# Performance work log

Measured on AMD Instinct MI355X. Metric: run time of the kernel, lower is better.

Reference implementation:

```python
import jax, jax.numpy as jnp
import numpy as np
import math

Q_SHAPES = [(20, 30), (10, 15), (5, 8)]
S_SHAPES = [(20, 30), (10, 15), (5, 8)]
C_IN = 256
C_OUT = 256
NUM_HEADS = 8


def _rel_indices(q_shapes, s_shapes):
    # Faithful translation of QSGA.get_rel_indices: block matrix over pyramid levels.
    rows = []
    for hq, wq in q_shapes:
        cols = []
        for hs, ws in s_shapes:
            ind = np.arange(ws)[None, :] / ws - np.arange(hq)[:, None] / hq  # [hq, ws]
            sc = math.sqrt(ws * hq)
            indx = np.tile(ind, (wq, hs)) * sc                              # [hq*wq, hs*ws]
            indy = np.repeat(np.repeat(ind, wq, axis=0), hs, axis=1) * sc   # [hq*wq, hs*ws]
            indd = indx ** 2 + indy ** 2
            cols.append(np.stack([indd, indx, indy], axis=-1))
        rows.append(np.concatenate(cols, axis=1))
    return jnp.asarray(np.concatenate(rows, axis=0)[None].astype(np.float32))  # [1, Nq, Ns, 3]


def setup_inputs() -> dict:
    key = jax.random.key(0)
    ks = jax.random.split(key, 8)
    B, M = 2, 5
    Nq = sum(h * w for h, w in Q_SHAPES)
    Ns = sum(h * w for h, w in S_SHAPES)
    std = 0.02
    # local_init: v = identity, pos_proj weight zero except col0 = -alphas, gating = ones
    min_a, max_a = 0.002, 0.2
    alphas = np.array([min_a + (max_a - min_a) / NUM_HEADS ** 2.5 * i ** 2.5 for i in range(NUM_HEADS)], np.float32)
    Wp = np.zeros((NUM_HEADS, 3), np.float32)
    Wp[:, 0] = -alphas
    return {
        "q_feat": jax.random.normal(ks[0], (B, Nq, C_IN), jnp.float32),
        "s_feat": jax.random.normal(ks[1], (M, Ns, C_IN), jnp.float32),
        "rel_indices": _rel_indices(Q_SHAPES, S_SHAPES),
        "Wq": jax.random.normal(ks[2], (C_OUT, C_IN), jnp.float32) * std,
        "bq": jnp.zeros((C_OUT,), jnp.float32),
        "Wk": jax.random.normal(ks[3], (C_OUT, C_IN), jnp.float32) * std,
        "bk": jnp.zeros((C_OUT,), jnp.float32),
        "Wv": jnp.eye(C_OUT, C_IN, dtype=jnp.float32),
        "bv": jnp.zeros((C_OUT,), jnp.float32),
        "Wp": jnp.asarray(Wp),
        "bp": jnp.zeros((NUM_HEADS,), jnp.float32),
        "Wo": jax.random.normal(ks[4], (C_OUT, C_OUT), jnp.float32) * std,
        "bo": jnp.zeros((C_OUT,), jnp.float32),
        "gating": jnp.ones((NUM_HEADS,), jnp.float32),
    }


def reference(q_feat, s_feat, rel_indices, Wq, bq, Wk, bk, Wv, bv, Wp, bp, Wo, bo, gating):
    B, Nq, _ = q_feat.shape
    M, Ns, _ = s_feat.shape
    H = gating.shape[0]
    C = Wq.shape[0]
    Dh = C // H
    scale = Dh ** -0.5
    # projections -> [B,H,Nq,Dh], [M,H,Ns,Dh]
    q = (q_feat @ Wq.T + bq).reshape(B, Nq, H, Dh).transpose(0, 2, 1, 3)
    k = (s_feat @ Wk.T + bk).reshape(M, Ns, H, Dh).transpose(0, 2, 1, 3)
    # content scores over all (query image, support image) pairs: [B,M,H,Nq,Ns]
    patch = jnp.einsum('bhqd,mhsd->bmhqs', q, k) * scale
    patch = jax.nn.softmax(patch, axis=-1)
    # positional scores: [1,Nq,Ns,3] -> [1,H,Nq,Ns]
    pos = jax.nn.softmax((rel_indices @ Wp.T + bp).transpose(0, 3, 1, 2), axis=-1)
    g = jax.nn.sigmoid(gating)[None, None, :, None, None]  # [1,1,H,1,1]
    attn = (1.0 - g) * patch + g * pos[:, None]            # broadcast pos over B,M
    attn = attn / attn.sum(axis=-1, keepdims=True)
    v = (s_feat @ Wv.T + bv).reshape(M, Ns, H, Dh).transpose(0, 2, 1, 3)  # [M,H,Ns,Dh]
    out = jnp.einsum('bmhqs,mhsd->bmhqd', attn, v)          # [B,M,H,Nq,Dh]
    out = out.transpose(0, 1, 3, 2, 4).reshape(B, M, Nq, C)  # [B,M,Nq,C]
    return out @ Wo.T + bo
```

## Files before the change

### kernel.cpp

```cpp
#include <hip/hip_runtime.h>
#include <hip/hip_bf16.h>
#include <math.h>

#define B_ 2
#define M_ 5
#define H_ 8
#define C_ 256
#define DH 32
#define NQ 790
#define NS 790
#define QT32 25
#define VROW 800
#define PPAD 800

typedef __attribute__((ext_vector_type(8))) __bf16 bf16x8;
typedef __attribute__((ext_vector_type(16))) float f32x16;
typedef unsigned int u32;
typedef unsigned short u16;

#define LOG2E 1.4426950408889634f

static __device__ __forceinline__ u16 bf16bits(float v) {
  union { __bf16 h; u16 u; } x; x.h = (__bf16)v; return x.u;
}
static __device__ __forceinline__ u32 pack2bf(float a, float b) {
  union { __bf16 h[2]; u32 u; } x; x.h[0] = (__bf16)a; x.h[1] = (__bf16)b; return x.u;
}

#define POS_N 395
#define GEMM0 395
#define PADBLK 544

#define PROJ_STEP(ACC, BY)                                                 \
  {                                                                        \
    int bcol_ = (BY) * 64 + wc * 32 + lo;                                  \
    const float* wf_ = Wm + (size_t)bcol_ * C_ + k0;                       \
    float4 g0_ = *(const float4*)wf_, g1_ = *(const float4*)(wf_ + 4);     \
    bf16x8 b_;                                                             \
    b_[0]=(__bf16)g0_.x; b_[1]=(__bf16)g0_.y; b_[2]=(__bf16)g0_.z; b_[3]=(__bf16)g0_.w; \
    b_[4]=(__bf16)g1_.x; b_[5]=(__bf16)g1_.y; b_[6]=(__bf16)g1_.z; b_[7]=(__bf16)g1_.w; \
    ACC = __builtin_amdgcn_mfma_f32_32x32x16_bf16(a_, b_, ACC, 0, 0, 0);   \
  }

#define STORE_QK(ACC, BY)                                                  \
  {                                                                        \
    int bcol_ = (BY) * 64 + wc * 32 + lo;                                  \
    float bvv_ = bias[bcol_];                                              \
    _Pragma("unroll")                                                      \
    for (int r_ = 0; r_ < 16; ++r_) {                                      \
      int row_ = (r_ & 3) + 8 * (r_ >> 2) + 4 * hi;                        \
      int grow_ = grow0 + wr * 32 + row_;                                  \
      if (grow_ < R) {                                                     \
        float v_ = (ACC[r_] + bvv_) * scale;                               \
        int seg_ = grow_ / 790, srow_ = grow_ - seg_ * 790;                \
        size_t addr_ = ((size_t)(seg_ * H_ + (bcol_ >> 5)) * 790 + srow_) * 32 + (bcol_ & 31); \
        outp[addr_] = bf16bits(v_);                                        \
      }                                                                    \
    }                                                                      \
  }

#define STORE_V(ACC, BY)                                                   \
  {                                                                        \
    int bcol_ = (BY) * 64 + wc * 32 + lo;                                  \
    float bvv_ = bias[bcol_];                                              \
    int cIn_ = wc * 32 + lo;                                               \
    _Pragma("unroll")                                                      \
    for (int r_ = 0; r_ < 16; ++r_) {                                      \
      int row_ = (r_ & 3) + 8 * (r_ >> 2) + 4 * hi;                        \
      Tls[cIn_][wr * 32 + row_] = bf16bits(ACC[r_] + bvv_);                \
    }                                                                      \
    __syncthreads();                                                       \
    {                                                                      \
      int c_l = tid >> 2, g_l = (tid & 3) * 16;                            \
      int gcol = (BY) * 64 + c_l;                                          \
      int g0v = grow0 + g_l;                                               \
      u16 vals_[16];                                                       \
      _Pragma("unroll")                                                    \
      for (int i_ = 0; i_ < 16; ++i_) vals_[i_] = Tls[c_l][g_l + i_];      \
      int mA_ = g0v / 790, mB_ = (g0v + 15) / 790;                         \
      u16* dst_ = vT2 + (size_t)gcol * (M_ * VROW);                        \
      if (mB_ < M_ && mA_ == mB_) {                                        \
        size_t base_ = (size_t)mA_ * VROW + (g0v - mA_ * 790);             \
        *(uint4*)(dst_ + base_)     = *(uint4*)(vals_);                    \
        *(uint4*)(dst_ + base_ + 8) = *(uint4*)(vals_ + 8);                \
      } else {                                                             \
        _Pragma("unroll")                                                  \
        for (int i_ = 0; i_ < 16; ++i_) {                                  \
          int g_ = g0v + i_;                                               \
          if (g_ < M_ * 790) {                                             \
            int mm_ = g_ / 790, ss_ = g_ - mm_ * 790;                      \
            dst_[(size_t)mm_ * VROW + ss_] = vals_[i_];                    \
          }                                                                \
        }                                                                  \
      }                                                                    \
    }                                                                      \
    __syncthreads();                                                       \
  }

__global__ __launch_bounds__(256) void stage1(const float* __restrict__ qf,
    const float* __restrict__ sf, const float* __restrict__ rel,
    const float* __restrict__ Wq, const float* __restrict__ bq,
    const float* __restrict__ Wk, const float* __restrict__ bk,
    const float* __restrict__ Wv, const float* __restrict__ bv,
    const float* __restrict__ Wp, const float* __restrict__ bp,
    u16* __restrict__ qb, u16* __restrict__ kb, u16* __restrict__ vT2,
    u16* __restrict__ pp, float qscale) {
  __shared__ u16 Tls[64][72];
  int bid = blockIdx.x;
  int tid = threadIdx.x;

  if (bid < POS_N) {
    int wave = tid >> 6, lane = tid & 63;
    int q = bid * 2 + (wave >> 1);
    int h0 = (wave & 1) * 4;
    float rd[13], rx[13], ry[13];
#pragma unroll
    for (int t = 0; t < 13; ++t) {
      int s = lane + 64 * t;
      if (s < NS) {
        const float* rp = rel + ((size_t)q * NS + s) * 3;
        rd[t] = rp[0]; rx[t] = rp[1]; ry[t] = rp[2];
      } else { rd[t] = 0.f; rx[t] = 0.f; ry[t] = 0.f; }
    }
    for (int h = h0; h < h0 + 4; ++h) {
      float w0 = Wp[h * 3] * LOG2E, w1 = Wp[h * 3 + 1] * LOG2E,
            w2 = Wp[h * 3 + 2] * LOG2E, b = bp[h] * LOG2E;
      float lg[13], mx = -1e30f;
#pragma unroll
      for (int t = 0; t < 13; ++t) {
        int s = lane + 64 * t;
        float v = rd[t] * w0 + rx[t] * w1 + ry[t] * w2 + b;
        lg[t] = (s < NS) ? v : -1e30f;
        mx = fmaxf(mx, lg[t]);
      }
#pragma unroll
      for (int off = 32; off; off >>= 1) mx = fmaxf(mx, __shfl_xor(mx, off));
      float sm = 0.f;
#pragma unroll
      for (int t = 0; t < 13; ++t) { lg[t] = exp2f(lg[t] - mx); sm += lg[t]; }
#pragma unroll
      for (int off = 32; off; off >>= 1) sm += __shfl_xor(sm, off);
      float inv = 1.f / sm;
#pragma unroll
      for (int t = 0; t < 13; ++t) {
        int s = lane + 64 * t;
        if (s < PPAD)
          pp[((size_t)h * NQ + q) * PPAD + s] = (s < NS) ? bf16bits(lg[t] * inv) : (u16)0;
      }
    }
    return;
  }

  if (bid == PADBLK) {
    int c = tid;
#pragma unroll
    for (int m = 0; m < M_; ++m) {
      u32* p = (u32*)(vT2 + (size_t)c * (M_ * VROW) + m * VROW + 790);
#pragma unroll
      for (int i = 0; i < 5; ++i) p[i] = 0;
    }
    return;
  }

  int j = bid - GEMM0;
  const float* A; const float* Wm; const float* bias; int R; float scale; int role; int bx;
  if (j < 25)      { A = qf; Wm = Wq; bias = bq; R = B_ * NQ; scale = qscale; role = 0; bx = j; }
  else if (j < 87) { A = sf; Wm = Wk; bias = bk; R = M_ * NS; scale = 1.f;    role = 1; bx = j - 25; }
  else             { A = sf; Wm = Wv; bias = bv; R = M_ * NS; scale = 1.f;    role = 2; bx = j - 87; }

  int wave = tid >> 6, lane = tid & 63;
  int lo = lane & 31, hi = lane >> 5;
  int wr = wave >> 1, wc = wave & 1;
  int grow0 = bx * 64;
  int arow = grow0 + wr * 32 + lo;
  int ar = arow < R ? arow : R - 1;

  f32x16 acc0, acc1, acc2, acc3;
#pragma unroll
  for (int r = 0; r < 16; ++r) { acc0[r] = 0.f; acc1[r] = 0.f; acc2[r] = 0.f; acc3[r] = 0.f; }
#pragma unroll
  for (int kk = 0; kk < 16; ++kk) {
    int k0 = kk * 16 + hi * 8;
    const float* af = A + (size_t)ar * C_ + k0;
    float4 f0 = *(const float4*)af, f1 = *(const float4*)(af + 4);
    bf16x8 a_;
    a_[0]=(__bf16)f0.x; a_[1]=(__bf16)f0.y; a_[2]=(__bf16)f0.z; a_[3]=(__bf16)f0.w;
    a_[4]=(__bf16)f1.x; a_[5]=(__bf16)f1.y; a_[6]=(__bf16)f1.z; a_[7]=(__bf16)f1.w;
    PROJ_STEP(acc0, 0);
    PROJ_STEP(acc1, 1);
    PROJ_STEP(acc2, 2);
    PROJ_STEP(acc3, 3);
  }

  if (role < 2) {
    u16* outp = (role == 0) ? qb : kb;
    STORE_QK(acc0, 0);
    STORE_QK(acc1, 1);
    STORE_QK(acc2, 2);
    STORE_QK(acc3, 3);
  } else {
    STORE_V(acc0, 0);
    STORE_V(acc1, 1);
    STORE_V(acc2, 2);
    STORE_V(acc3, 3);
  }
}

static __device__ __forceinline__ void wave_range(int wave, int& st, int& en) {
  st = wave * 6 + (wave ? 1 : 0);
  en = st + (wave ? 6 : 7);
}

#define SM_PV(c_, OACC, ZR, FV0, FV1)                                      \
  {                                                                        \
    float p_[16];                                                          \
    _Pragma("unroll")                                                      \
    for (int r_ = 0; r_ < 16; ++r_) p_[r_] = exp2f(c_[r_]);                \
    float s0_ = p_[0]+p_[1],  s1_ = p_[2]+p_[3];                           \
    float s2_ = p_[4]+p_[5],  s3_ = p_[6]+p_[7];                           \
    float s4_ = p_[8]+p_[9],  s5_ = p_[10]+p_[11];                         \
    float s6_ = p_[12]+p_[13], s7_ = p_[14]+p_[15];                        \
    s0_ += s1_; s2_ += s3_; s4_ += s5_; s6_ += s7_;                        \
    s0_ += s2_; s4_ += s6_;                                                \
    float ts_ = s0_ + s4_;                                                 \
    { float xa_ = ts_, xb_ = ts_;                                          \
      asm("v_permlane32_swap_b32 %0, %1" : "+v"(xa_), "+v"(xb_));          \
      ZR += xa_ + xb_; }                                                   \
    u32 pk_[8];                                                            \
    _Pragma("unroll")                                                      \
    for (int t_ = 0; t_ < 8; ++t_) pk_[t_] = pack2bf(p_[2*t_], p_[2*t_+1]); \
    asm("v_permlane32_swap_b32 %0, %1" : "+v"(pk_[0]), "+v"(pk_[2]));      \
    asm("v_permlane32_swap_b32 %0, %1" : "+v"(pk_[1]), "+v"(pk_[3]));      \
    asm("v_permlane32_swap_b32 %0, %1" : "+v"(pk_[4]), "+v"(pk_[6]));      \
    asm("v_permlane32_swap_b32 %0, %1" : "+v"(pk_[5]), "+v"(pk_[7]));      \
    union { u32 u[4]; bf16x8 v; } pa_, pb_;                                \
    pa_.u[0] = pk_[0]; pa_.u[1] = pk_[1]; pa_.u[2] = pk_[2]; pa_.u[3] = pk_[3]; \
    pb_.u[0] = pk_[4]; pb_.u[1] = pk_[5]; pb_.u[2] = pk_[6]; pb_.u[3] = pk_[7]; \
    OACC = __builtin_amdgcn_mfma_f32_32x32x16_bf16(FV0, pa_.v, OACC, 0, 0, 0); \
    OACC = __builtin_amdgcn_mfma_f32_32x32x16_bf16(FV1, pb_.v, OACC, 0, 0, 0); \
  }

#define TILE_BODY(KC0,KC1,VC0,VC1,PC0,PC1, KN0,KN1,VN0,VN1,PN0,PN1, IT, NT) \
  {                                                                        \
    int srn_ = (NT) * 32 + lo; if (srn_ >= NS) srn_ = NS - 1;              \
    KN0 = *(const bf16x8*)(kbase + (size_t)srn_ * 32 + hi8);               \
    KN1 = *(const bf16x8*)(kbase + (size_t)srn_ * 32 + 16 + hi8);          \
    VN0 = *(const bf16x8*)(vbase + (NT) * 32 + hi8);                       \
    VN1 = *(const bf16x8*)(vbase + (NT) * 32 + 16 + hi8);                  \
    PN0 = *(const bf16x8*)(pbase + (NT) * 32 + hi8);                       \
    PN1 = *(const bf16x8*)(pbase + (NT) * 32 + 16 + hi8);                  \
    f32x16 c0_ = kZero, c1_ = kZero;                                       \
    c0_ = __builtin_amdgcn_mfma_f32_32x32x16_bf16(KC0, fq00, c0_, 0, 0, 0);\
    c0_ = __builtin_amdgcn_mfma_f32_32x32x16_bf16(KC1, fq01, c0_, 0, 0, 0);\
    c1_ = __builtin_amdgcn_mfma_f32_32x32x16_bf16(KC0, fq10, c1_, 0, 0, 0);\
    c1_ = __builtin_amdgcn_mfma_f32_32x32x16_bf16(KC1, fq11, c1_, 0, 0, 0);\
    Opos = __builtin_amdgcn_mfma_f32_32x32x16_bf16(VC0, PC0, Opos, 0, 0, 0);\
    Opos = __builtin_amdgcn_mfma_f32_32x32x16_bf16(VC1, PC1, Opos, 0, 0, 0);\
    if ((IT) == 24) {                                                      \
      _Pragma("unroll")                                                    \
      for (int r_ = 0; r_ < 16; ++r_) {                                    \
        int sl_ = (r_ & 3) + 8 * (r_ >> 2) + 4 * hi;                       \
        if (768 + sl_ >= NS) { c0_[r_] = -1e30f; c1_[r_] = -1e30f; }       \
      }                                                                    \
    }                                                                      \
    SM_PV(c0_, O0, Z0, VC0, VC1);                                          \
    SM_PV(c1_, O1, Z1, VC0, VC1);                                          \
  }

__global__ __launch_bounds__(256, 2) void attn2(const u16* __restrict__ qb,
    const u16* __restrict__ kb, const u16* __restrict__ vT2,
    const u16* __restrict__ pp, const float* __restrict__ gating,
    u16* __restrict__ opb) {
  int logical = (blockIdx.x & 7) * 125 + (blockIdx.x >> 3);
  int m  = logical % M_;
  int r2 = logical / M_;
  int qt = r2 % QT32;
  int h  = r2 / QT32;
  int tid = threadIdx.x;
  int wave = tid >> 6, lane = tid & 63;
  int lo = lane & 31, hi = lane >> 5, hi8 = hi * 8;
  int qg = qt * 32 + lo;
  int qc = qg < NQ ? qg : NQ - 1;

  const u16* qp0 = qb + ((size_t)(0 * H_ + h) * NQ + qc) * 32 + hi8;
  const u16* qp1 = qb + ((size_t)(1 * H_ + h) * NQ + qc) * 32 + hi8;
  bf16x8 fq00 = *(const bf16x8*)qp0;
  bf16x8 fq01 = *(const bf16x8*)(qp0 + 16);
  bf16x8 fq10 = *(const bf16x8*)qp1;
  bf16x8 fq11 = *(const bf16x8*)(qp1 + 16);
  const u16* kbase = kb + ((size_t)(m * H_ + h) * NS) * 32;
  const u16* vbase = vT2 + (size_t)(h * DH + lo) * (M_ * VROW) + m * VROW;
  const u16* pbase = pp + ((size_t)h * NQ + qc) * PPAD;

  f32x16 O0, O1, Opos, kZero;
#pragma unroll
  for (int r = 0; r < 16; ++r) { O0[r] = 0.f; O1[r] = 0.f; Opos[r] = 0.f; kZero[r] = 0.f; }
  float Z0 = 0.f, Z1 = 0.f;
  int st, en; wave_range(wave, st, en);

  bf16x8 ak0, ak1, av0, av1, ap0, ap1, bk0, bk1, bv0, bv1, bp0, bp1;
  {
    int sr0 = st * 32 + lo; if (sr0 >= NS) sr0 = NS - 1;
    ak0 = *(const bf16x8*)(kbase + (size_t)sr0 * 32 + hi8);
    ak1 = *(const bf16x8*)(kbase + (size_t)sr0 * 32 + 16 + hi8);
    av0 = *(const bf16x8*)(vbase + st * 32 + hi8);
    av1 = *(const bf16x8*)(vbase + st * 32 + 16 + hi8);
    ap0 = *(const bf16x8*)(pbase + st * 32 + hi8);
    ap1 = *(const bf16x8*)(pbase + st * 32 + 16 + hi8);
  }
  int it = st;
  while (it + 2 <= en) {
    TILE_BODY(ak0, ak1, av0, av1, ap0, ap1, bk0, bk1, bv0, bv1, bp0, bp1, it, it + 1);
    int nt2 = (it + 2 < en) ? it + 2 : it + 1;
    TILE_BODY(bk0, bk1, bv0, bv1, bp0, bp1, ak0, ak1, av0, av1, ap0, ap1, it + 1, nt2);
    it += 2;
  }
  if (it < en) TILE_BODY(ak0, ak1, av0, av1, ap0, ap1, bk0, bk1, bv0, bv1, bp0, bp1, it, it);

  __shared__ float Os[4][32][33];
  __shared__ float Zs[4][32];
  float g = 1.f / (1.f + __expf(-gating[h]));
  int d = tid & 31, qi = tid >> 5;
  float oc0[4], oc1[4];

#pragma unroll
  for (int r = 0; r < 16; ++r) {
    int dd = (r & 3) + 8 * (r >> 2) + 4 * hi;
    Os[wave][dd][lo] = O0[r];
  }
  if (hi == 0) Zs[wave][lo] = Z0;
  __syncthreads();
#pragma unroll
  for (int k = 0; k < 4; ++k) {
    int ql = qi + 8 * k;
    float zg = Zs[0][ql] + Zs[1][ql] + Zs[2][ql] + Zs[3][ql];
    float oc = Os[0][d][ql] + Os[1][d][ql] + Os[2][d][ql] + Os[3][d][ql];
    oc0[k] = (1.f - g) * oc / zg;
  }
  __syncthreads();

#pragma unroll
  for (int r = 0; r < 16; ++r) {
    int dd = (r & 3) + 8 * (r >> 2) + 4 * hi;
    Os[wave][dd][lo] = O1[r];
  }
  if (hi == 0) Zs[wave][lo] = Z1;
  __syncthreads();
#pragma unroll
  for (int k = 0; k < 4; ++k) {
    int ql = qi + 8 * k;
    float zg = Zs[0][ql] + Zs[1][ql] + Zs[2][ql] + Zs[3][ql];
    float oc = Os[0][d][ql] + Os[1][d][ql] + Os[2][d][ql] + Os[3][d][ql];
    oc1[k] = (1.f - g) * oc / zg;
  }
  __syncthreads();

#pragma unroll
  for (int r = 0; r < 16; ++r) {
    int dd = (r & 3) + 8 * (r >> 2) + 4 * hi;
    Os[wave][dd][lo] = Opos[r];
  }
  __syncthreads();
  u16* out0 = opb + ((size_t)(0 * M_ + m) * NQ) * C_ + h * DH + d;
  u16* out1 = opb + ((size_t)(1 * M_ + m) * NQ) * C_ + h * DH + d;
#pragma unroll
  for (int k = 0; k < 4; ++k) {
    int ql = qi + 8 * k;
    int qgl = qt * 32 + ql;
    if (qgl < NQ) {
      float op = Os[0][d][ql] + Os[1][d][ql] + Os[2][d][ql] + Os[3][d][ql];
      out0[(size_t)qgl * C_] = bf16bits(oc0[k] + g * op);
      out1[(size_t)qgl * C_] = bf16bits(oc1[k] + g * op);
    }
  }
}

__global__ __launch_bounds__(256) void out_gemm(const u16* __restrict__ Ap,
    const float* __restrict__ W, const float* __restrict__ bias,
    float* __restrict__ outp, int R) {
  int tid = threadIdx.x;
  int wave = tid >> 6, lane = tid & 63;
  int lo = lane & 31, hi = lane >> 5;
  int wr = wave >> 1, wc = wave & 1;
  int arow = blockIdx.x * 64 + wr * 32 + lo;
  int ar = arow < R ? arow : R - 1;
  int bcolA = blockIdx.y * 128 + wc * 32 + lo;
  int bcolB = bcolA + 64;
  f32x16 accA, accB;
#pragma unroll
  for (int r = 0; r < 16; ++r) { accA[r] = 0.f; accB[r] = 0.f; }
#pragma unroll
  for (int kk = 0; kk < 16; ++kk) {
    int k0 = kk * 16 + hi * 8;
    bf16x8 a = *(const bf16x8*)(Ap + (size_t)ar * C_ + k0);
    bf16x8 b;
    const float* wf = W + (size_t)bcolA * C_ + k0;
    float4 g0 = *(const float4*)wf, g1 = *(const float4*)(wf + 4);
    b[0]=(__bf16)g0.x; b[1]=(__bf16)g0.y; b[2]=(__bf16)g0.z; b[3]=(__bf16)g0.w;
    b[4]=(__bf16)g1.x; b[5]=(__bf16)g1.y; b[6]=(__bf16)g1.z; b[7]=(__bf16)g1.w;
    accA = __builtin_amdgcn_mfma_f32_32x32x16_bf16(a, b, accA, 0, 0, 0);
    const float* wf2 = W + (size_t)bcolB * C_ + k0;
    float4 h0 = *(const float4*)wf2, h1 = *(const float4*)(wf2 + 4);
    b[0]=(__bf16)h0.x; b[1]=(__bf16)h0.y; b[2]=(__bf16)h0.z; b[3]=(__bf16)h0.w;
    b[4]=(__bf16)h1.x; b[5]=(__bf16)h1.y; b[6]=(__bf16)h1.z; b[7]=(__bf16)h1.w;
    accB = __builtin_amdgcn_mfma_f32_32x32x16_bf16(a, b, accB, 0, 0, 0);
  }
  float bvA = bias[bcolA], bvB = bias[bcolB];
#pragma unroll
  for (int r = 0; r < 16; ++r) {
    int row = (r & 3) + 8 * (r >> 2) + 4 * hi;
    int grow = blockIdx.x * 64 + wr * 32 + row;
    if (grow < R) {
      outp[(size_t)grow * C_ + bcolA] = accA[r] + bvA;
      outp[(size_t)grow * C_ + bcolB] = accB[r] + bvB;
    }
  }
}

extern "C" void kernel_launch(void* const* d_in, const int* in_sizes, int n_in,
                              void* d_out, int out_size, void* d_ws, size_t ws_size,
                              hipStream_t stream) {
  const float* q_feat = (const float*)d_in[0];
  const float* s_feat = (const float*)d_in[1];
  const float* rel    = (const float*)d_in[2];
  const float* Wq = (const float*)d_in[3];
  const float* bq = (const float*)d_in[4];
  const float* Wk = (const float*)d_in[5];
  const float* bk = (const float*)d_in[6];
  const float* Wv = (const float*)d_in[7];
  const float* bv = (const float*)d_in[8];
  const float* Wp = (const float*)d_in[9];
  const float* bp = (const float*)d_in[10];
  const float* Wo = (const float*)d_in[11];
  const float* bo = (const float*)d_in[12];
  const float* gating = (const float*)d_in[13];
  float* out = (float*)d_out;

  char* w = (char*)d_ws;
  u16* qb  = (u16*)w;
  u16* kb  = (u16*)(w + 808960);
  u16* vT2 = (u16*)(w + 2831360);
  u16* pp  = (u16*)(w + 4879360);
  u16* opb = (u16*)(w + 14991360);

  const float QSCALE = 0.17677669529663687f * 1.4426950408889634f;

  stage1<<<545, 256, 0, stream>>>(q_feat, s_feat, rel, Wq, bq, Wk, bk, Wv, bv,
                                  Wp, bp, qb, kb, vT2, pp, QSCALE);
  attn2<<<1000, 256, 0, stream>>>(qb, kb, vT2, pp, gating, opb);
  out_gemm<<<dim3(124, 2), 256, 0, stream>>>(opb, Wo, bo, out, B_ * M_ * NQ);
}
```

Measured before the change: 72.93 us.

## Drop register double-buffering in attention loop and raise occupancy to four blocks

```diff
diff --git a/kernel.cpp b/kernel.cpp
--- a/kernel.cpp
+++ b/kernel.cpp
@@ -125,19 +125,14 @@
     for (int h = h0; h < h0 + 4; ++h) {
       float w0 = Wp[h * 3] * LOG2E, w1 = Wp[h * 3 + 1] * LOG2E,
             w2 = Wp[h * 3 + 2] * LOG2E, b = bp[h] * LOG2E;
-      float lg[13], mx = -1e30f;
+      float lg[13], sm = 0.f;
 #pragma unroll
       for (int t = 0; t < 13; ++t) {
         int s = lane + 64 * t;
         float v = rd[t] * w0 + rx[t] * w1 + ry[t] * w2 + b;
-        lg[t] = (s < NS) ? v : -1e30f;
-        mx = fmaxf(mx, lg[t]);
+        lg[t] = exp2f((s < NS) ? v : -1e30f);
+        sm += lg[t];
       }
-#pragma unroll
-      for (int off = 32; off; off >>= 1) mx = fmaxf(mx, __shfl_xor(mx, off));
-      float sm = 0.f;
-#pragma unroll
-      for (int t = 0; t < 13; ++t) { lg[t] = exp2f(lg[t] - mx); sm += lg[t]; }
 #pragma unroll
       for (int off = 32; off; off >>= 1) sm += __shfl_xor(sm, off);
       float inv = 1.f / sm;
@@ -240,34 +235,7 @@
     OACC = __builtin_amdgcn_mfma_f32_32x32x16_bf16(FV1, pb_.v, OACC, 0, 0, 0); \
   }
 
-#define TILE_BODY(KC0,KC1,VC0,VC1,PC0,PC1, KN0,KN1,VN0,VN1,PN0,PN1, IT, NT) \
-  {                                                                        \
-    int srn_ = (NT) * 32 + lo; if (srn_ >= NS) srn_ = NS - 1;              \
-    KN0 = *(const bf16x8*)(kbase + (size_t)srn_ * 32 + hi8);               \
-    KN1 = *(const bf16x8*)(kbase + (size_t)srn_ * 32 + 16 + hi8);          \
-    VN0 = *(const bf16x8*)(vbase + (NT) * 32 + hi8);                       \
-    VN1 = *(const bf16x8*)(vbase + (NT) * 32 + 16 + hi8);                  \
-    PN0 = *(const bf16x8*)(pbase + (NT) * 32 + hi8);                       \
-    PN1 = *(const bf16x8*)(pbase + (NT) * 32 + 16 + hi8);                  \
-    f32x16 c0_ = kZero, c1_ = kZero;                                       \
-    c0_ = __builtin_amdgcn_mfma_f32_32x32x16_bf16(KC0, fq00, c0_, 0, 0, 0);\
-    c0_ = __builtin_amdgcn_mfma_f32_32x32x16_bf16(KC1, fq01, c0_, 0, 0, 0);\
-    c1_ = __builtin_amdgcn_mfma_f32_32x32x16_bf16(KC0, fq10, c1_, 0, 0, 0);\
-    c1_ = __builtin_amdgcn_mfma_f32_32x32x16_bf16(KC1, fq11, c1_, 0, 0, 0);\
-    Opos = __builtin_amdgcn_mfma_f32_32x32x16_bf16(VC0, PC0, Opos, 0, 0, 0);\
-    Opos = __builtin_amdgcn_mfma_f32_32x32x16_bf16(VC1, PC1, Opos, 0, 0, 0);\
-    if ((IT) == 24) {                                                      \
-      _Pragma("unroll")                                                    \
-      for (int r_ = 0; r_ < 16; ++r_) {                                    \
-        int sl_ = (r_ & 3) + 8 * (r_ >> 2) + 4 * hi;                       \
-        if (768 + sl_ >= NS) { c0_[r_] = -1e30f; c1_[r_] = -1e30f; }       \
-      }                                                                    \
-    }                                                                      \
-    SM_PV(c0_, O0, Z0, VC0, VC1);                                          \
-    SM_PV(c1_, O1, Z1, VC0, VC1);                                          \
-  }
-
-__global__ __launch_bounds__(256, 2) void attn2(const u16* __restrict__ qb,
+__global__ __launch_bounds__(256, 4) void attn2(const u16* __restrict__ qb,
     const u16* __restrict__ kb, const u16* __restrict__ vT2,
     const u16* __restrict__ pp, const float* __restrict__ gating,
     u16* __restrict__ opb) {
@@ -298,24 +266,33 @@
   float Z0 = 0.f, Z1 = 0.f;
   int st, en; wave_range(wave, st, en);
 
-  bf16x8 ak0, ak1, av0, av1, ap0, ap1, bk0, bk1, bv0, bv1, bp0, bp1;
-  {
-    int sr0 = st * 32 + lo; if (sr0 >= NS) sr0 = NS - 1;
-    ak0 = *(const bf16x8*)(kbase + (size_t)sr0 * 32 + hi8);
-    ak1 = *(const bf16x8*)(kbase + (size_t)sr0 * 32 + 16 + hi8);
-    av0 = *(const bf16x8*)(vbase + st * 32 + hi8);
-    av1 = *(const bf16x8*)(vbase + st * 32 + 16 + hi8);
-    ap0 = *(const bf16x8*)(pbase + st * 32 + hi8);
-    ap1 = *(const bf16x8*)(pbase + st * 32 + 16 + hi8);
-  }
-  int it = st;
-  while (it + 2 <= en) {
-    TILE_BODY(ak0, ak1, av0, av1, ap0, ap1, bk0, bk1, bv0, bv1, bp0, bp1, it, it + 1);
-    int nt2 = (it + 2 < en) ? it + 2 : it + 1;
-    TILE_BODY(bk0, bk1, bv0, bv1, bp0, bp1, ak0, ak1, av0, av1, ap0, ap1, it + 1, nt2);
-    it += 2;
-  }
-  if (it < en) TILE_BODY(ak0, ak1, av0, av1, ap0, ap1, bk0, bk1, bv0, bv1, bp0, bp1, it, it);
+  for (int it = st; it < en; ++it) {
+    int sr = it * 32 + lo; if (sr >= NS) sr = NS - 1;
+    bf16x8 kf0 = *(const bf16x8*)(kbase + (size_t)sr * 32 + hi8);
+    bf16x8 kf1 = *(const bf16x8*)(kbase + (size_t)sr * 32 + 16 + hi8);
+    bf16x8 vf0 = *(const bf16x8*)(vbase + it * 32 + hi8);
+    bf16x8 vf1 = *(const bf16x8*)(vbase + it * 32 + 16 + hi8);
+    bf16x8 pf0 = *(const bf16x8*)(pbase + it * 32 + hi8);
+    bf16x8 pf1 = *(const bf16x8*)(pbase + it * 32 + 16 + hi8);
+
+    f32x16 c0 = kZero, c1 = kZero;
+    c0 = __builtin_amdgcn_mfma_f32_32x32x16_bf16(kf0, fq00, c0, 0, 0, 0);
+    c0 = __builtin_amdgcn_mfma_f32_32x32x16_bf16(kf1, fq01, c0, 0, 0, 0);
+    c1 = __builtin_amdgcn_mfma_f32_32x32x16_bf16(kf0, fq10, c1, 0, 0, 0);
+    c1 = __builtin_amdgcn_mfma_f32_32x32x16_bf16(kf1, fq11, c1, 0, 0, 0);
+    Opos = __builtin_amdgcn_mfma_f32_32x32x16_bf16(vf0, pf0, Opos, 0, 0, 0);
+    Opos = __builtin_amdgcn_mfma_f32_32x32x16_bf16(vf1, pf1, Opos, 0, 0, 0);
+
+    if (it == 24) {
+#pragma unroll
+      for (int r = 0; r < 16; ++r) {
+        int sl = (r & 3) + 8 * (r >> 2) + 4 * hi;
+        if (768 + sl >= NS) { c0[r] = -1e30f; c1[r] = -1e30f; }
+      }
+    }
+    SM_PV(c0, O0, Z0, vf0, vf1);
+    SM_PV(c1, O1, Z1, vf0, vf1);
+  }
 
   __shared__ float Os[4][32][33];
   __shared__ float Zs[4][32];
```

Result: slower. 75.51 us (+3.5%).
